# Performance work log

Hardware: AMD Instinct MI355X
Metric: run time of the kernel (lower is better)

## Reference

```python
import jax, jax.numpy as jnp
import numpy as np

B = 4096          # number of comments
N_SRT = 8192      # number of subtitle hidden states
D_C = 768         # comment_hidden_size
D_S = 1024        # srt_hidden_size
K = 2             # k_hidden_states


def setup_inputs() -> dict:
    key = jax.random.key(0)
    k1, k2, k3, k4, k5, k6 = jax.random.split(key, 6)
    s = lambda d: 1.0 / np.sqrt(d)
    return {
        "hidden_states_srt": jax.random.normal(k1, (N_SRT, D_S), dtype=jnp.float32),
        "hidden_states_comments": jax.random.normal(k2, (B, D_C), dtype=jnp.float32),
        "W_comment": jax.random.uniform(k3, (D_C, D_S), jnp.float32, -s(D_C), s(D_C)),
        "b_comment": jax.random.uniform(k4, (D_S,), jnp.float32, -s(D_C), s(D_C)),
        "W_srt": jax.random.uniform(k5, (D_S, D_S), jnp.float32, -s(D_S), s(D_S)),
        "b_srt": jax.random.uniform(k6, (D_S,), jnp.float32, -s(D_S), s(D_S)),
        "k": K,
    }


def reference(hidden_states_srt, hidden_states_comments, W_comment, b_comment, W_srt, b_srt, k):
    # Linear + ReLU (dropout is identity in eval mode)
    transformed_comments = jax.nn.relu(hidden_states_comments @ W_comment + b_comment)  # [B, D_S]
    transformed_srt = jax.nn.relu(hidden_states_srt @ W_srt + b_srt)                    # [N, D_S]
    # Dense attention scores + softmax over srt dim
    attention_scores = transformed_comments @ transformed_srt.T                          # [B, N]
    attention_weights = jax.nn.softmax(attention_scores, axis=-1)
    # Top-k over srt dim; gather the corresponding transformed srt rows per batch element
    _, top_indices = jax.lax.top_k(attention_weights, k)                                 # [B, k]
    selected_states = transformed_srt[top_indices]                                       # [B, k, D_S]
    return selected_states
```

## Files before the change

kernel.cpp:

```cpp
#include <hip/hip_runtime.h>
#include <math.h>

#define B_C   4096
#define N_SRT 8192
#define D_C   768
#define D_S   1024
#define KSEL  2
#define NGRP  (N_SRT / 4)
#define PGRP  4

typedef float    f32x4  __attribute__((ext_vector_type(4)));
typedef short    short8 __attribute__((ext_vector_type(8)));
typedef _Float16 half8  __attribute__((ext_vector_type(8)));

__device__ inline unsigned short f2bf(float f) {
    unsigned u = __float_as_uint(f);
    u += 0x7FFF + ((u >> 16) & 1);
    return (unsigned short)(u >> 16);
}
__device__ inline float bf2f(unsigned short h) {
    return __uint_as_float(((unsigned)h) << 16);
}

#define GLOAD_LDS16(gsrc, ldst)                                                     \
    __builtin_amdgcn_global_load_lds(                                               \
        (const __attribute__((address_space(1))) void*)(gsrc),                      \
        (__attribute__((address_space(3))) void*)(ldst), 16, 0, 0)

#define WAIT_VM4  asm volatile("s_waitcnt vmcnt(4)" ::: "memory")
#define WAIT_VM0  asm volatile("s_waitcnt vmcnt(0)" ::: "memory")
#define WAIT_LGKM asm volatile("s_waitcnt lgkmcnt(0)" ::: "memory")

#define NS_ACT ((N_SRT * D_S / 8 + B_C * D_C / 8) / 256)

__global__ __launch_bounds__(256)
void split_all(const float* __restrict__ srt, const float* __restrict__ com,
               _Float16* __restrict__ pS, _Float16* __restrict__ pC,
               const float* __restrict__ Ws, _Float16* __restrict__ WtS,
               const float* __restrict__ Wc, _Float16* __restrict__ WtC) {
    __shared__ float t[64][65];
    if ((int)blockIdx.x < NS_ACT) {
        const int g = blockIdx.x * 256 + threadIdx.x;
        const int E0 = N_SRT * D_S / 8;
        const float* src;
        _Float16* dst;
        size_t stride;
        if (g < E0) {
            src = srt + (size_t)g * 8; dst = pS + (size_t)g * 8;
            stride = (size_t)N_SRT * D_S;
        } else {
            const int g2 = g - E0;
            src = com + (size_t)g2 * 8; dst = pC + (size_t)g2 * 8;
            stride = (size_t)B_C * D_C;
        }
        const float4 a = *reinterpret_cast<const float4*>(src);
        const float4 b = *reinterpret_cast<const float4*>(src + 4);
        const float x[8] = {a.x, a.y, a.z, a.w, b.x, b.y, b.z, b.w};
        half8 hv, mv;
#pragma unroll
        for (int j = 0; j < 8; ++j) {
            const _Float16 h = (_Float16)x[j];
            const float    r = x[j] - (float)h;
            hv[j] = h; mv[j] = (_Float16)(r * 2048.0f);
        }
        *reinterpret_cast<half8*>(dst)          = hv;
        *reinterpret_cast<half8*>(dst + stride) = mv;
    } else {
        const int bb = (int)blockIdx.x - NS_ACT;
        const bool p1 = bb >= 256;
        const int  b  = p1 ? bb - 256 : bb;
        const float* __restrict__ W = p1 ? Wc : Ws;
        _Float16* __restrict__ Wt   = p1 ? WtC : WtS;
        const int K  = p1 ? D_C : D_S;
        const int n0 = (b & 15) * 64, k0 = (b >> 4) * 64;

        const int tid = threadIdx.x;
        const int c = tid & 63, rq = tid >> 6;
#pragma unroll
        for (int j = 0; j < 16; ++j) {
            const int kr = rq * 16 + j;
            t[kr][c] = W[(size_t)(k0 + kr) * D_S + n0 + c];
        }
        __syncthreads();
        const size_t PS = (size_t)K * D_S;
#pragma unroll
        for (int j = 0; j < 16; ++j) {
            const int nr = rq * 16 + j;
            const float xs = t[c][nr] * 32768.0f;
            const _Float16 h = (_Float16)xs;
            const float    r = xs - (float)h;
            const size_t o = (size_t)(n0 + nr) * K + k0 + c;
            Wt[o]      = h;
            Wt[o + PS] = (_Float16)(r * 2048.0f);
        }
    }
}

__global__ __launch_bounds__(256)
void transform_mfma_all(const _Float16* __restrict__ actS,
                        const _Float16* __restrict__ wtS,
                        const float* __restrict__ bS,
                        float* __restrict__ CS, unsigned short* __restrict__ HS,
                        const _Float16* __restrict__ actC,
                        const _Float16* __restrict__ wtC,
                        const float* __restrict__ bC,
                        float* __restrict__ CC, unsigned short* __restrict__ HC) {
    __shared__ __align__(16) _Float16 sW[2][2][128 * 32];
    __shared__ __align__(16) _Float16 sA[2][2][128 * 32];
    const int tid  = threadIdx.x;
    const int lane = tid & 63;
    const int w    = tid >> 6;
    const int lr   = lane & 15, lg = lane >> 4;
    const int wn   = w & 1, wc = w >> 1;

    const int hw = blockIdx.x;
    int lgid, seg;
    if (hw < 512) { seg = 0; lgid = (hw & 7) * 64 + (hw >> 3); }
    else          { const int h2 = hw - 512; seg = 1; lgid = (h2 & 7) * 32 + (h2 >> 3); }

    const _Float16* __restrict__ actP = seg ? actC : actS;
    const _Float16* __restrict__ wtP  = seg ? wtC  : wtS;
    const float* __restrict__ bias    = seg ? bC   : bS;
    float* __restrict__ C             = seg ? CC   : CS;
    unsigned short* __restrict__ H    = seg ? HC   : HS;
    const int K   = seg ? D_C : D_S;
    const int NC  = seg ? (D_C / 32) : (D_S / 32);
    const size_t aps = seg ? (size_t)B_C * D_C : (size_t)N_SRT * D_S;
    const size_t wps = (size_t)D_S * K;

    const int bn = (lgid & 7) * 128;
    const int bm = (lgid >> 3) * 128;

    const f32x4 vzero = {0.f, 0.f, 0.f, 0.f};
    f32x4 acc[4][4];
#pragma unroll
    for (int i = 0; i < 4; ++i)
#pragma unroll
        for (int j = 0; j < 4; ++j) acc[i][j] = vzero;

    auto stage = [&](int buf, int c) {
        const int kb = c * 32;
#pragma unroll
        for (int i = 0; i < 2; ++i) {
            const int idx = tid + i * 256;
            const int r   = idx >> 2;
            const int sw  = ((idx & 3) ^ ((r >> 1) & 3)) * 8;
            const size_t wo = (size_t)(bn + r) * K + kb + sw;
            const size_t ao = (size_t)(bm + r) * K + kb + sw;
            GLOAD_LDS16(wtP  + wo,       (char*)&sW[buf][0][0] + idx * 16);
            GLOAD_LDS16(wtP  + wps + wo, (char*)&sW[buf][1][0] + idx * 16);
            GLOAD_LDS16(actP + ao,       (char*)&sA[buf][0][0] + idx * 16);
            GLOAD_LDS16(actP + aps + ao, (char*)&sA[buf][1][0] + idx * 16);
        }
    };

    stage(0, 0);
    WAIT_VM0;
    __builtin_amdgcn_s_barrier();

    for (int c = 0; c < NC; ++c) {
        const int cur = c & 1;
        if (c + 1 < NC) stage(cur ^ 1, c + 1);

        half8 a0[4], a1[4], b0[4], b1[4], b0s[4];
#pragma unroll
        for (int t4 = 0; t4 < 4; ++t4) {
            const int ra = wn * 64 + t4 * 16 + lr;
            const int oa = ra * 64 + ((lg ^ ((ra >> 1) & 3)) * 16);
            a0[t4] = *(const half8*)((const char*)&sW[cur][0][0] + oa);
            a1[t4] = *(const half8*)((const char*)&sW[cur][1][0] + oa);
            const int rb = wc * 64 + t4 * 16 + lr;
            const int ob = rb * 64 + ((lg ^ ((rb >> 1) & 3)) * 16);
            b0[t4] = *(const half8*)((const char*)&sA[cur][0][0] + ob);
            b1[t4] = *(const half8*)((const char*)&sA[cur][1][0] + ob);
            b0s[t4] = b0[t4] * (_Float16)2048.0f;
        }
        __builtin_amdgcn_s_setprio(1);
#pragma unroll
        for (int i = 0; i < 4; ++i)
#pragma unroll
            for (int j = 0; j < 4; ++j) {
                acc[i][j] = __builtin_amdgcn_mfma_f32_16x16x32_f16(
                    a0[i], b0s[j], acc[i][j], 0, 0, 0);
                acc[i][j] = __builtin_amdgcn_mfma_f32_16x16x32_f16(
                    a0[i], b1[j],  acc[i][j], 0, 0, 0);
                acc[i][j] = __builtin_amdgcn_mfma_f32_16x16x32_f16(
                    a1[i], b0[j],  acc[i][j], 0, 0, 0);
            }
        __builtin_amdgcn_s_setprio(0);

        WAIT_VM0;
        WAIT_LGKM;
        __builtin_amdgcn_s_barrier();
    }

    const float s2 = 1.4901161193847656e-8f;
#pragma unroll
    for (int i = 0; i < 4; ++i) {
        const int n = bn + wn * 64 + i * 16 + lg * 4;
        const f32x4 bb = *reinterpret_cast<const f32x4*>(&bias[n]);
#pragma unroll
        for (int j = 0; j < 4; ++j) {
            const int m = bm + wc * 64 + j * 16 + lr;
            f32x4 o;
#pragma unroll
            for (int q = 0; q < 4; ++q)
                o[q] = fmaxf(fmaf(acc[i][j][q], s2, bb[q]), 0.f);
            *reinterpret_cast<f32x4*>(&C[(size_t)m * D_S + n]) = o;
            ushort4 hh;
            hh.x = f2bf(o[0]); hh.y = f2bf(o[1]);
            hh.z = f2bf(o[2]); hh.w = f2bf(o[3]);
            *reinterpret_cast<ushort4*>(&H[(size_t)m * D_S + n]) = hh;
        }
    }
}

#define NB0 ((B_C / 128) * (D_S / 128))
#define NB1 ((N_SRT / 128) * (D_S / 128))

__global__ __launch_bounds__(256)
void transform_fused(const float* __restrict__ A0, const float* __restrict__ W0,
                     const float* __restrict__ b0, float* __restrict__ C0,
                     unsigned short* __restrict__ H0,
                     const float* __restrict__ A1, const float* __restrict__ W1,
                     const float* __restrict__ b1, float* __restrict__ C1,
                     unsigned short* __restrict__ H1) {
    __shared__ __align__(16) float As[2][128][16];
    __shared__ __align__(16) float Bs[2][2048];

    const bool p1 = (int)blockIdx.x >= NB0;
    const int  b  = p1 ? (int)blockIdx.x - NB0 : (int)blockIdx.x;
    const float* __restrict__ A = p1 ? A1 : A0;
    const float* __restrict__ W = p1 ? W1 : W0;
    const float* __restrict__ bias = p1 ? b1 : b0;
    float* __restrict__ C = p1 ? C1 : C0;
    unsigned short* __restrict__ H = p1 ? H1 : H0;
    const int K = p1 ? D_S : D_C;

    const int bn = (b & 7) * 128;
    const int bm = (b >> 3) * 128;

    const int tid = threadIdx.x;
    const int tx = tid & 15, ty = tid >> 4;

    int a_off[2], w_off[2];
#pragma unroll
    for (int i = 0; i < 2; ++i) {
        const int idx = tid + i * 256;
        const int r = idx >> 2, q = idx & 3;
        a_off[i] = r * K + (q ^ ((r >> 3) & 3)) * 4;
        const int s = idx & 63;
        const int kloc = 2 * (idx >> 6) + ((s >> 4) & 1);
        const int cb   = 2 * (s & 15) + (s >> 5);
        w_off[i] = kloc * D_S + cb * 4;
    }

#define STAGE(bufi, k0)                                                        \
    {                                                                          \
        _Pragma("unroll")                                                      \
        for (int i = 0; i < 2; ++i) {                                          \
            const int idx = tid + i * 256;                                     \
            GLOAD_LDS16(A + (size_t)bm * K + (k0) + a_off[i],                  \
                        (char*)&As[bufi][0][0] + idx * 16);                    \
            GLOAD_LDS16(W + (size_t)(k0) * D_S + bn + w_off[i],                \
                        (char*)&Bs[bufi][0] + idx * 16);                       \
        }                                                                      \
    }

    float acc[8][8] = {};

    STAGE(0, 0);
    __syncthreads();

    const int nk = K / 16;
    for (int t = 0; t < nk; ++t) {
        const int cur = t & 1;
        if (t + 1 < nk) STAGE(t & 1 ? 0 : 1, (t + 1) * 16);

        const float* __restrict__ Bf = &Bs[cur][0];
#pragma unroll
        for (int kq = 0; kq < 4; ++kq) {
            f32x4 a4[8];
#pragma unroll
            for (int i = 0; i < 8; ++i)
                a4[i] = *reinterpret_cast<const f32x4*>(
                    &As[cur][ty * 8 + i][(kq ^ (ty & 3)) * 4]);
#pragma unroll
            for (int k2 = 0; k2 < 4; ++k2) {
                const int k = kq * 4 + k2;
                const int boff = (k >> 1) * 256 + (tx + ((k & 1) << 4)) * 4;
                const f32x4 bx = *reinterpret_cast<const f32x4*>(Bf + boff);
                const f32x4 by = *reinterpret_cast<const f32x4*>(Bf + boff + 128);
                const float bv[8] = {bx[0], bx[1], bx[2], bx[3], by[0], by[1], by[2], by[3]};
#pragma unroll
                for (int i = 0; i < 8; ++i) {
                    const float av = a4[i][k2];
#pragma unroll
                    for (int j = 0; j < 8; ++j)
                        acc[i][j] = fmaf(av, bv[j], acc[i][j]);
                }
            }
        }
        __syncthreads();
    }
#undef STAGE

    const f32x4 g0 = *reinterpret_cast<const f32x4*>(&bias[bn + tx * 8]);
    const f32x4 g1 = *reinterpret_cast<const f32x4*>(&bias[bn + tx * 8 + 4]);
#pragma unroll
    for (int i = 0; i < 8; ++i) {
        const int m = bm + ty * 8 + i;
        const int n = bn + tx * 8;
        f32x4 o0, o1;
#pragma unroll
        for (int j = 0; j < 4; ++j) {
            o0[j] = fmaxf(acc[i][j]     + g0[j], 0.f);
            o1[j] = fmaxf(acc[i][j + 4] + g1[j], 0.f);
        }
        *reinterpret_cast<f32x4*>(&C[(size_t)m * D_S + n])     = o0;
        *reinterpret_cast<f32x4*>(&C[(size_t)m * D_S + n + 4]) = o1;
        short8 h;
#pragma unroll
        for (int j = 0; j < 4; ++j) {
            h[j]     = (short)f2bf(o0[j]);
            h[j + 4] = (short)f2bf(o1[j]);
        }
        *reinterpret_cast<short8*>(&H[(size_t)m * D_S + n]) = h;
    }
}

__global__ __launch_bounds__(512)
void scores_filter(const unsigned short* __restrict__ TSh,
                   const unsigned short* __restrict__ TCh,
                   float* __restrict__ part) {
    __shared__ __align__(16) unsigned short sA[2][2][128 * 64];
    __shared__ __align__(16) unsigned short sB[2][2][128 * 64];
    const int tid  = threadIdx.x;
    const int lane = tid & 63;
    const int w    = tid >> 6;
    const int mw   = w >> 2;
    const int nw   = w & 3;
    const int bh   = nw >> 1;
    const int lr   = lane & 15, lg = lane >> 4;

    const int hw   = blockIdx.x;
    const int lgid = (hw & 7) * 64 + (hw >> 3);
    const int n0   = (lgid & 31) * 256;
    const int c0   = (lgid >> 5) * 256;

    const f32x4 vzero = {0.f, 0.f, 0.f, 0.f};
    f32x4 acc[8][4];
#pragma unroll
    for (int i = 0; i < 8; ++i)
#pragma unroll
        for (int j = 0; j < 4; ++j) acc[i][j] = vzero;

    auto stageHalf = [&](unsigned short* ldsbase, const unsigned short* grow0,
                         int kb) {
#pragma unroll
        for (int i = 0; i < 2; ++i) {
            const int idx = tid + i * 512;
            const int r   = idx >> 3;
            const int sw  = ((idx & 7) ^ (r & 7)) * 8;
            GLOAD_LDS16(grow0 + (size_t)r * D_S + kb + sw,
                        (char*)ldsbase + idx * 16);
        }
    };

    const unsigned short* TS0 = TSh + (size_t)n0 * D_S;
    const unsigned short* TS1 = TSh + (size_t)(n0 + 128) * D_S;
    const unsigned short* TC0 = TCh + (size_t)c0 * D_S;
    const unsigned short* TC1 = TCh + (size_t)(c0 + 128) * D_S;

    stageHalf(&sA[0][0][0], TS0, 0);
    stageHalf(&sA[0][1][0], TS1, 0);
    stageHalf(&sB[0][0][0], TC0, 0);
    stageHalf(&sB[0][1][0], TC1, 0);
    stageHalf(&sB[1][0][0], TC0, 64);
    stageHalf(&sB[1][1][0], TC1, 64);
    WAIT_VM4;
    __builtin_amdgcn_s_barrier();

    const int NITER = D_S / 128;
    for (int t = 0; t < NITER; ++t) {
        const bool nl = (t + 1 < NITER);

#pragma unroll
        for (int par = 0; par < 2; ++par) {
            short8 bfr[4][2];
#pragma unroll
            for (int ph = 0; ph < 4; ++ph) {
                short8 afr[2][2];
                if (ph == 0) {
#pragma unroll
                    for (int j = 0; j < 4; ++j) {
                        const int rb = (nw & 1) * 64 + j * 16 + lr;
#pragma unroll
                        for (int kk = 0; kk < 2; ++kk)
                            bfr[j][kk] = *(const short8*)(
                                (const char*)&sB[par][bh][0] + rb * 128 +
                                (((kk * 4 + lg) ^ (rb & 7)) * 16));
                    }
                }
#pragma unroll
                for (int ii = 0; ii < 2; ++ii) {
                    const int ra = (ph * 2 + ii) * 16 + lr;
#pragma unroll
                    for (int kk = 0; kk < 2; ++kk)
                        afr[ii][kk] = *(const short8*)(
                            (const char*)&sA[par][mw][0] + ra * 128 +
                            (((kk * 4 + lg) ^ (ra & 7)) * 16));
                }
                if (par == 0) {
                    if (ph == 0)            stageHalf(&sA[1][0][0], TS0, (2*t+1)*64);
                    else if (ph == 1)       stageHalf(&sA[1][1][0], TS1, (2*t+1)*64);
                    else if (ph == 2) { if (nl) stageHalf(&sB[0][0][0], TC0, (2*t+2)*64); }
                    else              { if (nl) stageHalf(&sB[0][1][0], TC1, (2*t+2)*64); }
                } else {
                    if (ph == 0)      { if (nl) stageHalf(&sA[0][0][0], TS0, (2*t+2)*64); }
                    else if (ph == 1) { if (nl) stageHalf(&sA[0][1][0], TS1, (2*t+2)*64); }
                    else if (ph == 2) { if (nl) stageHalf(&sB[1][0][0], TC0, (2*t+3)*64); }
                    else              { if (nl) stageHalf(&sB[1][1][0], TC1, (2*t+3)*64); }
                }
                if (ph == 3) { if (nl) { WAIT_VM4; } else { WAIT_VM0; } }
                __builtin_amdgcn_s_barrier();
                WAIT_LGKM;
                __builtin_amdgcn_s_setprio(1);
#pragma unroll
                for (int ii = 0; ii < 2; ++ii)
#pragma unroll
                    for (int j = 0; j < 4; ++j)
#pragma unroll
                        for (int kk = 0; kk < 2; ++kk)
                            acc[ph * 2 + ii][j] = __builtin_amdgcn_mfma_f32_16x16x32_bf16(
                                afr[ii][kk], bfr[j][kk], acc[ph * 2 + ii][j], 0, 0, 0);
                __builtin_amdgcn_s_setprio(0);
                __builtin_amdgcn_s_barrier();
            }
        }
    }

    const int gbase = (n0 >> 2) + mw * 32;
#pragma unroll
    for (int j = 0; j < 4; ++j) {
        float v1 = -INFINITY, v2 = -INFINITY;
        int   g1 = 0, g2 = 0;
#pragma unroll
        for (int i = 0; i < 8; ++i) {
            const f32x4 v = acc[i][j];
            const float m = fmaxf(fmaxf(v.x, v.y), fmaxf(v.z, v.w));
            const int g = gbase + i * 4 + lg;
            if (m > v1)      { v2 = v1; g2 = g1; v1 = m; g1 = g; }
            else if (m > v2) { v2 = m; g2 = g; }
        }
#pragma unroll
        for (int off = 16; off <= 32; off <<= 1) {
            const float ov1 = __shfl_xor(v1, off);
            const int   og1 = __shfl_xor(g1, off);
            const float ov2 = __shfl_xor(v2, off);
            const int   og2 = __shfl_xor(g2, off);
            if (ov1 > v1 || (ov1 == v1 && og1 < g1)) { v2 = v1; g2 = g1; v1 = ov1; g1 = og1; }
            else if (ov1 > v2 || (ov1 == v2 && og1 < g2)) { v2 = ov1; g2 = og1; }
            if (ov2 > v1 || (ov2 == v1 && og2 < g1)) { v2 = v1; g2 = g1; v1 = ov2; g1 = og2; }
            else if (ov2 > v2 || (ov2 == v2 && og2 < g2)) { v2 = ov2; g2 = og2; }
        }
        if (lg == 0) {
            const int c = c0 + nw * 64 + j * 16 + lr;
            const int blk2 = (lgid & 31) * 2 + mw;
            f32x4 e;
            e[0] = v1; e[1] = __int_as_float(g1);
            e[2] = v2; e[3] = __int_as_float(g2);
            *reinterpret_cast<f32x4*>(&part[((size_t)c * 64 + blk2) * 4]) = e;
        }
    }
}

__global__ __launch_bounds__(256)
void refine_gather(const float* __restrict__ t_c, const float* __restrict__ t_s,
                   const float* __restrict__ part, float* __restrict__ out) {
    __shared__ float tc[D_S];
    __shared__ float sc[4 * PGRP];
    __shared__ int   selg[PGRP];
    __shared__ int   sel[2];
    const int row = blockIdx.x;
    const int tid = threadIdx.x;
    *reinterpret_cast<float4*>(&tc[tid * 4]) =
        *reinterpret_cast<const float4*>(&t_c[(size_t)row * D_S + tid * 4]);
    const int w = tid >> 6, lane = tid & 63;

    if (w == 0) {
        const f32x4 e = *reinterpret_cast<const f32x4*>(
            &part[((size_t)row * 64 + lane) * 4]);
        const float v[2]  = {e[0], e[2]};
        const int   gi[2] = {__float_as_int(e[1]), __float_as_int(e[3])};
        float pv = INFINITY; int pi = -1;
        int gl[PGRP];
#pragma unroll
        for (int k = 0; k < PGRP; ++k) {
            float bv = -INFINITY; int bi = 0x7FFFFFFF;
#pragma unroll
            for (int s = 0; s < 2; ++s) {
                const bool after  = (v[s] < pv) || (v[s] == pv && gi[s] > pi);
                const bool before = (v[s] > bv) || (v[s] == bv && gi[s] < bi);
                if (after && before) { bv = v[s]; bi = gi[s]; }
            }
#pragma unroll
            for (int off = 32; off >= 1; off >>= 1) {
                const float ov = __shfl_xor(bv, off);
                const int   oi = __shfl_xor(bi, off);
                if ((ov > bv) || (ov == bv && oi < bi)) { bv = ov; bi = oi; }
            }
            gl[k] = bi; pv = bv; pi = bi;
        }
#pragma unroll
        for (int a = 0; a < PGRP; ++a)
#pragma unroll
            for (int b2 = 0; b2 < PGRP - 1; ++b2)
                if (gl[b2] > gl[b2 + 1]) { int t = gl[b2]; gl[b2] = gl[b2 + 1]; gl[b2 + 1] = t; }
        if (lane == 0) {
#pragma unroll
            for (int k = 0; k < PGRP; ++k) selg[k] = gl[k];
        }
    }
    __syncthreads();

    float4 c4[4];
#pragma unroll
    for (int q = 0; q < 4; ++q)
        c4[q] = *reinterpret_cast<const float4*>(&tc[lane * 16 + q * 4]);
    const int g = selg[w];
#pragma unroll
    for (int o = 0; o < 4; ++o) {
        const int n = g * 4 + o;
        const float* ts = t_s + (size_t)n * D_S + lane * 16;
        float p = 0.f;
#pragma unroll
        for (int q = 0; q < 4; ++q) {
            const float4 tv = *reinterpret_cast<const float4*>(ts + q * 4);
            p += c4[q].x * tv.x + c4[q].y * tv.y + c4[q].z * tv.z + c4[q].w * tv.w;
        }
#pragma unroll
        for (int off = 32; off >= 1; off >>= 1) p += __shfl_xor(p, off);
        if (lane == 0) sc[w * 4 + o] = p;
    }
    __syncthreads();
    if (tid == 0) {
        float v1 = -INFINITY, v2 = -INFINITY; int i1 = 0, i2 = 0;
#pragma unroll
        for (int s = 0; s < 4 * PGRP; ++s) {
            const int n = selg[s >> 2] * 4 + (s & 3);
            const float v = sc[s];
            if (v > v1)      { v2 = v1; i2 = i1; v1 = v; i1 = n; }
            else if (v > v2) { v2 = v; i2 = n; }
        }
        sel[0] = i1; sel[1] = i2;
    }
    __syncthreads();
#pragma unroll
    for (int q = 0; q < 2; ++q) {
        const int src = sel[q];
        const float4 v = *reinterpret_cast<const float4*>(
            &t_s[(size_t)src * D_S + tid * 4]);
        *reinterpret_cast<float4*>(
            &out[((size_t)row * KSEL + q) * D_S + tid * 4]) = v;
    }
}

extern "C" void kernel_launch(void* const* d_in, const int* in_sizes, int n_in,
                              void* d_out, int out_size, void* d_ws, size_t ws_size,
                              hipStream_t stream) {
    const float* srt      = (const float*)d_in[0];
    const float* comments = (const float*)d_in[1];
    const float* Wc       = (const float*)d_in[2];
    const float* bc       = (const float*)d_in[3];
    const float* Ws       = (const float*)d_in[4];
    const float* bs       = (const float*)d_in[5];
    float* out = (float*)d_out;

    char* p = (char*)d_ws;
    float* t_c = (float*)p;          p += (size_t)B_C * D_S * 4;
    float* t_s = (float*)p;          p += (size_t)N_SRT * D_S * 4;
    unsigned short* tc_h = (unsigned short*)p; p += (size_t)B_C * D_S * 2;
    unsigned short* ts_h = (unsigned short*)p; p += (size_t)N_SRT * D_S * 2;
    float* part = (float*)p;         p += (size_t)B_C * NGRP * 2;
    p += (size_t)B_C * PGRP * 4;
    p += (size_t)B_C * KSEL * 4;

    _Float16* actS = (_Float16*)p; p += 2 * (size_t)N_SRT * D_S * 2;
    _Float16* actC = (_Float16*)p; p += 2 * (size_t)B_C * D_C * 2;
    _Float16* wtS  = (_Float16*)p; p += 2 * (size_t)D_S * D_S * 2;
    _Float16* wtC  = (_Float16*)p; p += 2 * (size_t)D_S * D_C * 2;
    const size_t required = (size_t)(p - (char*)d_ws);

    if (ws_size >= required) {
        split_all<<<NS_ACT + 448, 256, 0, stream>>>(
            srt, comments, actS, actC, Ws, wtS, Wc, wtC);

        transform_mfma_all<<<512 + 256, 256, 0, stream>>>(
            actS, wtS, bs, t_s, ts_h,
            actC, wtC, bc, t_c, tc_h);
    } else {
        transform_fused<<<NB0 + NB1, 256, 0, stream>>>(
            comments, Wc, bc, t_c, tc_h,
            srt,      Ws, bs, t_s, ts_h);
    }

    scores_filter<<<512, 512, 0, stream>>>(ts_h, tc_h, part);
    refine_gather<<<B_C, 256, 0, stream>>>(t_c, t_s, part, out);
}
```

Before: 217.1 us.

## Restructure split-fp16 transform GEMM into 512-thread 8-phase pipelined kernel

Replaces the 256-thread 128x128-tile transform GEMM with a 512-thread kernel that computes a 256x128 tile. The three split-precision products (hi*hi scaled, hi*lo, lo*hi) are serialised as separate K passes with 64-wide K steps, instead of being done as three MFMAs per fragment. Each K tile is split into four phases that interleave LDS fragment reads, asynchronous global-to-LDS staging of the next weight and activation tiles, and MFMAs, using partial vmcnt waits. The aim is to overlap memory transfer with compute and raise weight reuse. The cost is many more barriers per tile and higher register and LDS pressure.

```diff
diff --git a/kernel.cpp b/kernel.cpp
--- a/kernel.cpp
+++ b/kernel.cpp
@@ -28,6 +28,7 @@
         (__attribute__((address_space(3))) void*)(ldst), 16, 0, 0)
 
 #define WAIT_VM4  asm volatile("s_waitcnt vmcnt(4)" ::: "memory")
+#define WAIT_VM2  asm volatile("s_waitcnt vmcnt(2)" ::: "memory")
 #define WAIT_VM0  asm volatile("s_waitcnt vmcnt(0)" ::: "memory")
 #define WAIT_LGKM asm volatile("s_waitcnt lgkmcnt(0)" ::: "memory")
 
@@ -96,40 +97,46 @@
     }
 }
 
-__global__ __launch_bounds__(256)
-void transform_mfma_all(const _Float16* __restrict__ actS,
-                        const _Float16* __restrict__ wtS,
-                        const float* __restrict__ bS,
-                        float* __restrict__ CS, unsigned short* __restrict__ HS,
-                        const _Float16* __restrict__ actC,
-                        const _Float16* __restrict__ wtC,
-                        const float* __restrict__ bC,
-                        float* __restrict__ CC, unsigned short* __restrict__ HC) {
-    __shared__ __align__(16) _Float16 sW[2][2][128 * 32];
-    __shared__ __align__(16) _Float16 sA[2][2][128 * 32];
+__global__ __launch_bounds__(512)
+void transform_8ph(const _Float16* __restrict__ actS,
+                   const _Float16* __restrict__ wtS,
+                   const float* __restrict__ bS,
+                   float* __restrict__ CS, unsigned short* __restrict__ HS,
+                   const _Float16* __restrict__ actC,
+                   const _Float16* __restrict__ wtC,
+                   const float* __restrict__ bC,
+                   float* __restrict__ CC, unsigned short* __restrict__ HC) {
+    __shared__ __align__(16) _Float16 sW[2][2][128 * 64];
+    __shared__ __align__(16) _Float16 sAct[2][2][64 * 64];
     const int tid  = threadIdx.x;
     const int lane = tid & 63;
     const int w    = tid >> 6;
+    const int mw2  = w >> 1;
+    const int nb   = w & 1;
+    const int mh   = mw2 >> 1;
     const int lr   = lane & 15, lg = lane >> 4;
-    const int wn   = w & 1, wc = w >> 1;
 
     const int hw = blockIdx.x;
     int lgid, seg;
-    if (hw < 512) { seg = 0; lgid = (hw & 7) * 64 + (hw >> 3); }
-    else          { const int h2 = hw - 512; seg = 1; lgid = (h2 & 7) * 32 + (h2 >> 3); }
+    if (hw < 256) { seg = 0; lgid = (hw & 7) * 32 + (hw >> 3); }
+    else          { const int h2 = hw - 256; seg = 1; lgid = (h2 & 7) * 16 + (h2 >> 3); }
 
     const _Float16* __restrict__ actP = seg ? actC : actS;
     const _Float16* __restrict__ wtP  = seg ? wtC  : wtS;
     const float* __restrict__ bias    = seg ? bC   : bS;
     float* __restrict__ C             = seg ? CC   : CS;
     unsigned short* __restrict__ H    = seg ? HC   : HS;
-    const int K   = seg ? D_C : D_S;
-    const int NC  = seg ? (D_C / 32) : (D_S / 32);
+    const int K    = seg ? D_C : D_S;
+    const int NT   = seg ? 36 : 48;
+    const int NIT  = NT >> 1;
     const size_t aps = seg ? (size_t)B_C * D_C : (size_t)N_SRT * D_S;
     const size_t wps = (size_t)D_S * K;
 
-    const int bn = (lgid & 7) * 128;
-    const int bm = (lgid >> 3) * 128;
+    const int bn = (lgid & 3) * 256;
+    const int m0 = (lgid >> 2) * 128;
+
+    auto ppOf = [&](int tt) { return seg ? ((tt >= 12) + (tt >= 24)) : (tt >> 4); };
+    auto kbOf = [&](int tt, int pp) { return seg ? (tt - pp * 12) * 64 : ((tt & 15) * 64); };
 
     const f32x4 vzero = {0.f, 0.f, 0.f, 0.f};
     f32x4 acc[4][4];
@@ -138,70 +145,107 @@
 #pragma unroll
         for (int j = 0; j < 4; ++j) acc[i][j] = vzero;
 
-    auto stage = [&](int buf, int c) {
-        const int kb = c * 32;
+    auto stageW = [&](int buf, int half, int tt) {
+        const int pp = ppOf(tt); const int kb = kbOf(tt, pp);
+        const _Float16* g = wtP + (pp == 2 ? wps : 0)
+                          + (size_t)(bn + half * 128) * K + kb;
 #pragma unroll
         for (int i = 0; i < 2; ++i) {
-            const int idx = tid + i * 256;
-            const int r   = idx >> 2;
-            const int sw  = ((idx & 3) ^ ((r >> 1) & 3)) * 8;
-            const size_t wo = (size_t)(bn + r) * K + kb + sw;
-            const size_t ao = (size_t)(bm + r) * K + kb + sw;
-            GLOAD_LDS16(wtP  + wo,       (char*)&sW[buf][0][0] + idx * 16);
-            GLOAD_LDS16(wtP  + wps + wo, (char*)&sW[buf][1][0] + idx * 16);
-            GLOAD_LDS16(actP + ao,       (char*)&sA[buf][0][0] + idx * 16);
-            GLOAD_LDS16(actP + aps + ao, (char*)&sA[buf][1][0] + idx * 16);
+            const int idx = tid + i * 512;
+            const int r   = idx >> 3;
+            const int sw  = ((idx & 7) ^ (r & 7)) * 8;
+            GLOAD_LDS16(g + (size_t)r * K + sw,
+                        (char*)&sW[buf][half][0] + idx * 16);
         }
     };
-
-    stage(0, 0);
-    WAIT_VM0;
+    auto stageA = [&](int buf, int half, int tt) {
+        const int pp = ppOf(tt); const int kb = kbOf(tt, pp);
+        const _Float16* g = actP + (pp == 1 ? aps : 0)
+                          + (size_t)(m0 + half * 64) * K + kb;
+        const int idx = tid;
+        const int r   = idx >> 3;
+        const int sw  = ((idx & 7) ^ (r & 7)) * 8;
+        GLOAD_LDS16(g + (size_t)r * K + sw,
+                    (char*)&sAct[buf][half][0] + idx * 16);
+    };
+
+    stageW(0, 0, 0); stageW(0, 1, 0);
+    stageA(0, 0, 0); stageA(0, 1, 0);
+    stageA(1, 0, 1); stageA(1, 1, 1);
+    WAIT_VM2;
     __builtin_amdgcn_s_barrier();
 
-    for (int c = 0; c < NC; ++c) {
-        const int cur = c & 1;
-        if (c + 1 < NC) stage(cur ^ 1, c + 1);
-
-        half8 a0[4], a1[4], b0[4], b1[4], b0s[4];
-#pragma unroll
-        for (int t4 = 0; t4 < 4; ++t4) {
-            const int ra = wn * 64 + t4 * 16 + lr;
-            const int oa = ra * 64 + ((lg ^ ((ra >> 1) & 3)) * 16);
-            a0[t4] = *(const half8*)((const char*)&sW[cur][0][0] + oa);
-            a1[t4] = *(const half8*)((const char*)&sW[cur][1][0] + oa);
-            const int rb = wc * 64 + t4 * 16 + lr;
-            const int ob = rb * 64 + ((lg ^ ((rb >> 1) & 3)) * 16);
-            b0[t4] = *(const half8*)((const char*)&sA[cur][0][0] + ob);
-            b1[t4] = *(const half8*)((const char*)&sA[cur][1][0] + ob);
-            b0s[t4] = b0[t4] * (_Float16)2048.0f;
-        }
-        __builtin_amdgcn_s_setprio(1);
-#pragma unroll
-        for (int i = 0; i < 4; ++i)
-#pragma unroll
-            for (int j = 0; j < 4; ++j) {
-                acc[i][j] = __builtin_amdgcn_mfma_f32_16x16x32_f16(
-                    a0[i], b0s[j], acc[i][j], 0, 0, 0);
-                acc[i][j] = __builtin_amdgcn_mfma_f32_16x16x32_f16(
-                    a0[i], b1[j],  acc[i][j], 0, 0, 0);
-                acc[i][j] = __builtin_amdgcn_mfma_f32_16x16x32_f16(
-                    a1[i], b0[j],  acc[i][j], 0, 0, 0);
+    for (int it = 0; it < NIT; ++it) {
+        const bool nl = (it + 1 < NIT);
+#pragma unroll
+        for (int par = 0; par < 2; ++par) {
+            const int tt = 2 * it + par;
+            const bool sc = (ppOf(tt) == 0);
+            half8 bfr[4][2];
+#pragma unroll
+            for (int ph = 0; ph < 4; ++ph) {
+                half8 afr[2];
+                if (ph == 0) {
+#pragma unroll
+                    for (int j = 0; j < 4; ++j) {
+                        const int rb = j * 16 + lr;
+#pragma unroll
+                        for (int ks = 0; ks < 2; ++ks)
+                            bfr[j][ks] = *(const half8*)(
+                                (const char*)&sAct[par][nb][0] + rb * 128 +
+                                (((ks * 4 + lg) ^ (rb & 7)) * 16));
+                    }
+                    if (sc) {
+#pragma unroll
+                        for (int j = 0; j < 4; ++j)
+#pragma unroll
+                            for (int ks = 0; ks < 2; ++ks)
+                                bfr[j][ks] = bfr[j][ks] * (_Float16)2048.0f;
+                    }
+                }
+                {
+                    const int ra = (mw2 & 1) * 64 + ph * 16 + lr;
+#pragma unroll
+                    for (int ks = 0; ks < 2; ++ks)
+                        afr[ks] = *(const half8*)(
+                            (const char*)&sW[par][mh][0] + ra * 128 +
+                            (((ks * 4 + lg) ^ (ra & 7)) * 16));
+                }
+                if (par == 0) {
+                    if (ph == 0)            stageW(1, 0, tt + 1);
+                    else if (ph == 1)       stageW(1, 1, tt + 1);
+                    else if (ph == 2) { if (nl) stageA(0, 0, tt + 2); }
+                    else              { if (nl) stageA(0, 1, tt + 2); }
+                } else {
+                    if (ph == 0)      { if (nl) stageW(0, 0, tt + 1); }
+                    else if (ph == 1) { if (nl) stageW(0, 1, tt + 1); }
+                    else if (ph == 2) { if (nl) stageA(1, 0, tt + 2); }
+                    else              { if (nl) stageA(1, 1, tt + 2); }
+                }
+                if (ph == 3) { if (nl) { WAIT_VM2; } else { WAIT_VM0; } }
+                __builtin_amdgcn_s_barrier();
+                WAIT_LGKM;
+                __builtin_amdgcn_s_setprio(1);
+#pragma unroll
+                for (int j = 0; j < 4; ++j)
+#pragma unroll
+                    for (int ks = 0; ks < 2; ++ks)
+                        acc[ph][j] = __builtin_amdgcn_mfma_f32_16x16x32_f16(
+                            afr[ks], bfr[j][ks], acc[ph][j], 0, 0, 0);
+                __builtin_amdgcn_s_setprio(0);
+                __builtin_amdgcn_s_barrier();
             }
-        __builtin_amdgcn_s_setprio(0);
-
-        WAIT_VM0;
-        WAIT_LGKM;
-        __builtin_amdgcn_s_barrier();
+        }
     }
 
     const float s2 = 1.4901161193847656e-8f;
 #pragma unroll
     for (int i = 0; i < 4; ++i) {
-        const int n = bn + wn * 64 + i * 16 + lg * 4;
+        const int n = bn + mw2 * 64 + i * 16 + lg * 4;
         const f32x4 bb = *reinterpret_cast<const f32x4*>(&bias[n]);
 #pragma unroll
         for (int j = 0; j < 4; ++j) {
-            const int m = bm + wc * 64 + j * 16 + lr;
+            const int m = m0 + nb * 64 + j * 16 + lr;
             f32x4 o;
 #pragma unroll
             for (int q = 0; q < 4; ++q)
@@ -596,7 +640,7 @@
         split_all<<<NS_ACT + 448, 256, 0, stream>>>(
             srt, comments, actS, actC, Ws, wtS, Wc, wtC);
 
-        transform_mfma_all<<<512 + 256, 256, 0, stream>>>(
+        transform_8ph<<<256 + 128, 512, 0, stream>>>(
             actS, wtS, bs, t_s, ts_h,
             actC, wtC, bc, t_c, tc_h);
     } else {
```

Result: slower. 241.3 us (+11.2%).
